# Kernel optimization log

Hardware: AMD Instinct MI355X
Metric: run time of the kernel (lower is better)

Reference implementation:

```python
import jax, jax.numpy as jnp
import numpy as np

B, N, DIM, HEADS, DEPTH, MLP = 4, 1024, 256, 4, 4, 1024
DH = DIM // HEADS
EPS = 1e-5


def _ln(x, g, b):
    mu = jnp.mean(x, axis=-1, keepdims=True)
    var = jnp.mean((x - mu) ** 2, axis=-1, keepdims=True)
    return (x - mu) / jnp.sqrt(var + EPS) * g + b


def setup_inputs() -> dict:
    key = jax.random.key(0)
    ks = jax.random.split(key, 10)
    s = 0.02
    p = {}
    p["x"] = jax.random.normal(ks[0], (B, N, DIM), jnp.float32)
    p["attn_bias"] = jax.random.normal(ks[1], (2, B, HEADS, N, N), jnp.float32)
    p["ln1_g"] = jnp.ones((DEPTH, DIM), jnp.float32)
    p["ln1_b"] = jnp.zeros((DEPTH, DIM), jnp.float32)
    p["Wkv"] = jax.random.normal(ks[2], (DEPTH, DIM, 2 * DIM), jnp.float32) * s
    p["Wq"] = jax.random.normal(ks[3], (DEPTH, DIM, DIM), jnp.float32) * s
    p["Wo"] = jax.random.normal(ks[4], (DEPTH, DIM, DIM), jnp.float32) * s
    p["bo"] = jnp.zeros((DEPTH, DIM), jnp.float32)
    p["ln2_g"] = jnp.ones((DEPTH, DIM), jnp.float32)
    p["ln2_b"] = jnp.zeros((DEPTH, DIM), jnp.float32)
    p["W1"] = jax.random.normal(ks[5], (DEPTH, DIM, MLP), jnp.float32) * s
    p["b1"] = jnp.zeros((DEPTH, MLP), jnp.float32)
    p["W2"] = jax.random.normal(ks[6], (DEPTH, MLP, DIM), jnp.float32) * s
    p["b2"] = jnp.zeros((DEPTH, DIM), jnp.float32)
    p["Wg"] = jax.random.normal(ks[7], (DIM, DIM), jnp.float32) * s
    p["lng_g"] = jnp.ones((DIM,), jnp.float32)
    p["lng_b"] = jnp.zeros((DIM,), jnp.float32)
    return p


def reference(x, attn_bias, ln1_g, ln1_b, Wkv, Wq, Wo, bo, ln2_g, ln2_b, W1, b1, W2, b2, Wg, lng_g, lng_b):
    scale = DIM ** -0.5
    add_attn = attn_bias[0] + attn_bias[1]            # [B,H,N,N]
    # aggregation bias matrices are layer-invariant (recomputed identically each layer in torch)
    A = jnp.mean(attn_bias[0], axis=1)                # [B,N,N]
    S = jnp.mean(attn_bias[1], axis=1)
    G = jax.nn.softmax(A * S, axis=2)                 # [B,N,N]

    def split_heads(t):  # [B,N,DIM] -> [B,H,N,DH]
        return t.reshape(B, N, HEADS, DH).transpose(0, 2, 1, 3)

    for l in range(DEPTH):
        # softmax-GCN aggregation
        x_ma = jax.nn.relu(_ln(jnp.matmul(G, x) @ Wg, lng_g, lng_b))
        # attention (PreNorm on x only; q comes from un-normed x_ma)
        xn = _ln(x, ln1_g[l], ln1_b[l])
        kv = xn @ Wkv[l]
        k, v = jnp.split(kv, 2, axis=-1)
        q = x_ma @ Wq[l]
        qh, kh, vh = split_heads(q), split_heads(k), split_heads(v)
        dots = jnp.einsum('bhid,bhjd->bhij', qh, kh) * scale + add_attn
        attn = jax.nn.softmax(dots, axis=-1)
        out = jnp.einsum('bhij,bhjd->bhid', attn, vh)
        out = out.transpose(0, 2, 1, 3).reshape(B, N, DIM)
        x = x + out @ Wo[l] + bo[l]
        # feed-forward (exact GELU, matching torch nn.GELU default)
        xn2 = _ln(x, ln2_g[l], ln2_b[l])
        x = x + jax.nn.gelu(xn2 @ W1[l] + b1[l], approximate=False) @ W2[l] + b2[l]
    return x
```

## Files before the change

### kernel.cpp

```cpp
#include <hip/hip_runtime.h>
#include <hip/hip_bf16.h>
#include <math.h>

typedef unsigned short u16;
typedef __bf16 bf16x8 __attribute__((ext_vector_type(8)));
typedef float f32x4 __attribute__((ext_vector_type(4)));

#define B_ 4
#define N_ 1024
#define DIM_ 256
#define HEADS_ 4
#define DH_ 64
#define MLP_ 1024
#define DEPTH_ 4

__device__ __forceinline__ float r2f(u16 r){ return __uint_as_float(((unsigned)r)<<16); }
__device__ __forceinline__ u16 f2r(float f){ __hip_bfloat16 h = __float2bfloat16(f); return *(u16*)&h; }
__device__ __forceinline__ void stv(float* p, float v){ *p = v; }
__device__ __forceinline__ void stv(u16* p, float v){ *p = f2r(v); }

__device__ __forceinline__ float gelu_exact(float v){
  return 0.5f*v*(1.0f + erff(v*0.70710678118654752440f));
}

#define MFMA16(a,b,c) __builtin_amdgcn_mfma_f32_16x16x32_bf16(a,b,c,0,0,0)

__global__ void prep_bias(const float* __restrict__ bias, u16* __restrict__ G, u16* __restrict__ bsum){
  int blk = blockIdx.x;
  int i = blk & (N_-1);
  int b = blk >> 10;
  int t = threadIdx.x;
  __shared__ float sc[N_];
  __shared__ float red[256];
  long long base0 = ((long long)(b*HEADS_)*N_ + i)*(long long)N_;
  const long long hs = (long long)N_*N_;
  const long long cs = (long long)B_*HEADS_*N_*N_;
  float lmax = -3e38f;
  for (int jj=0;jj<4;jj++){
    int j = t + jj*256;
    float a = 0.f, s = 0.f;
    #pragma unroll
    for (int h=0;h<HEADS_;h++){
      float x0 = bias[base0 + h*hs + j];
      float x1 = bias[cs + base0 + h*hs + j];
      a += x0; s += x1;
      bsum[base0 + h*hs + j] = f2r(x0 + x1);
    }
    float v = (a*0.25f)*(s*0.25f);
    sc[j] = v;
    lmax = fmaxf(lmax, v);
  }
  red[t]=lmax; __syncthreads();
  for (int s=128;s>0;s>>=1){ if(t<s) red[t]=fmaxf(red[t],red[t+s]); __syncthreads(); }
  float m = red[0]; __syncthreads();
  float lsum = 0.f;
  for (int jj=0;jj<4;jj++){
    int j = t + jj*256;
    float e = __expf(sc[j]-m);
    sc[j]=e; lsum+=e;
  }
  red[t]=lsum; __syncthreads();
  for (int s=128;s>0;s>>=1){ if(t<s) red[t]+=red[t+s]; __syncthreads(); }
  float inv = 1.0f/red[0];
  u16* Grow = G + ((long long)b*N_ + i)*(long long)N_;
  for (int jj=0;jj<4;jj++){ int j=t+jj*256; Grow[j]=f2r(sc[j]*inv); }
}

__global__ void ln_kernel(const float* __restrict__ X, u16* __restrict__ Y,
                          const float* __restrict__ g, const float* __restrict__ bvec){
  int row = blockIdx.x, t = threadIdx.x;
  __shared__ float red[256];
  float v = X[(long long)row*DIM_ + t];
  red[t]=v; __syncthreads();
  for (int s=128;s>0;s>>=1){ if(t<s) red[t]+=red[t+s]; __syncthreads(); }
  float mu = red[0]*(1.0f/DIM_); __syncthreads();
  float d = v - mu;
  red[t]=d*d; __syncthreads();
  for (int s=128;s>0;s>>=1){ if(t<s) red[t]+=red[t+s]; __syncthreads(); }
  float var = red[0]*(1.0f/DIM_);
  Y[(long long)row*DIM_ + t] = f2r(d*rsqrtf(var+1e-5f)*g[t] + bvec[t]);
}

__global__ void tcast_all(const float* __restrict__ Wkv, const float* __restrict__ Wq,
                          const float* __restrict__ Wo, const float* __restrict__ W1,
                          const float* __restrict__ W2, const float* __restrict__ Wg,
                          const float* __restrict__ xin,
                          u16* WkvT, u16* WqT, u16* WoT, u16* W1T, u16* W2T, u16* WgT, u16* xT){
  int z = blockIdx.z;
  const float* I; u16* O; int ldin, R, C;
  if (z < 4)       { I = Wkv + z*131072;      O = WkvT + z*131072;      ldin=512;  R=256;  C=512;  }
  else if (z < 8)  { I = Wq  + (z-4)*65536;   O = WqT  + (z-4)*65536;   ldin=256;  R=256;  C=256;  }
  else if (z < 12) { I = Wo  + (z-8)*65536;   O = WoT  + (z-8)*65536;   ldin=256;  R=256;  C=256;  }
  else if (z < 16) { I = W1  + (z-12)*262144; O = W1T  + (z-12)*262144; ldin=1024; R=256;  C=1024; }
  else if (z < 20) { I = W2  + (z-16)*262144; O = W2T  + (z-16)*262144; ldin=256;  R=1024; C=256;  }
  else if (z == 20){ I = Wg;                  O = WgT;                  ldin=256;  R=256;  C=256;  }
  else             { I = xin + (z-21)*262144; O = xT   + (z-21)*262144; ldin=256;  R=1024; C=256;  }
  int c0 = blockIdx.x*32, r0 = blockIdx.y*32;
  if (c0 >= C || r0 >= R) return;
  __shared__ float tile[32][33];
  int tx = threadIdx.x, ty = threadIdx.y;
  #pragma unroll
  for (int i=0;i<4;i++)
    tile[ty*4+i][tx] = I[(long long)(r0+ty*4+i)*ldin + c0+tx];
  __syncthreads();
  #pragma unroll
  for (int i=0;i<4;i++)
    O[(long long)(c0+ty*4+i)*R + r0+tx] = f2r(tile[tx][ty*4+i]);
}

template<typename OT, int ACT>
__global__ __launch_bounds__(256) void wgemm(
    const u16* __restrict__ A, const u16* __restrict__ BT, OT* __restrict__ Cb,
    int K, int lda, int ldbt, int ldc, int ZS,
    long long sAb, long long sAh, long long sBb, long long sBh,
    long long sCb, long long sCh,
    const float* __restrict__ colBias, const float* __restrict__ res,
    u16* __restrict__ vt)
{
  int z = blockIdx.z, zb = z>>ZS, zh = z & ((1<<ZS)-1);
  A  += zb*sAb + zh*sAh;
  BT += zb*sBb + zh*sBh;
  long long co = zb*sCb + zh*sCh;
  int tid = threadIdx.x, w = tid>>6, lane = tid&63;
  int lr = lane&15, qd = lane>>4;
  int m0 = blockIdx.y*64 + (w>>1)*32;
  int n0 = blockIdx.x*64 + (w&1)*32;
  const u16* Ap0 = A  + (long long)(m0+lr)*lda;
  const u16* Ap1 = A  + (long long)(m0+16+lr)*lda;
  const u16* Bp0 = BT + (long long)(n0+lr)*ldbt;
  const u16* Bp1 = BT + (long long)(n0+16+lr)*ldbt;
  f32x4 acc[2][2] = {};
  for (int k0=0; k0<K; k0+=64){
    #pragma unroll
    for (int ks=0; ks<2; ks++){
      int ko = k0 + ks*32 + qd*8;
      bf16x8 a0 = *(const bf16x8*)(Ap0+ko);
      bf16x8 a1 = *(const bf16x8*)(Ap1+ko);
      bf16x8 b0 = *(const bf16x8*)(Bp0+ko);
      bf16x8 b1 = *(const bf16x8*)(Bp1+ko);
      acc[0][0] = MFMA16(a0,b0,acc[0][0]);
      acc[0][1] = MFMA16(a0,b1,acc[0][1]);
      acc[1][0] = MFMA16(a1,b0,acc[1][0]);
      acc[1][1] = MFMA16(a1,b1,acc[1][1]);
    }
  }
  OT* C = Cb + co;
  const float* rs = res ? res + co : nullptr;
  #pragma unroll
  for (int rt=0;rt<2;rt++){
    #pragma unroll
    for (int ct=0;ct<2;ct++){
      int gc = n0 + ct*16 + lr;
      float cb = colBias ? colBias[gc] : 0.f;
      #pragma unroll
      for (int r=0;r<4;r++){
        int gr = m0 + rt*16 + qd*4 + r;
        float v = acc[rt][ct][r] + cb;
        if (ACT) v = gelu_exact(v);
        if (rs) v += rs[(long long)gr*ldc + gc];
        stv(C + (long long)gr*ldc + gc, v);
        if (vt && gc >= 256){
          int b = gr>>10, rl = gr&1023;
          vt[(long long)b*262144 + (long long)(gc-256)*1024 + rl] = f2r(v);
        }
      }
    }
  }
}

static inline void gemm(hipStream_t st, const u16* A, const u16* BT, void* C, int outBf, int act,
    int M, int N, int K, int lda, int ldbt, int ldc, int Z, int ZS,
    long long sAb, long long sAh, long long sBb, long long sBh, long long sCb, long long sCh,
    const float* cb, const float* res, u16* vt)
{
  dim3 g(N/64, M/64, Z), b(256);
  if (outBf){
    if (act) wgemm<u16,1><<<g,b,0,st>>>(A,BT,(u16*)C,K,lda,ldbt,ldc,ZS,sAb,sAh,sBb,sBh,sCb,sCh,cb,res,vt);
    else     wgemm<u16,0><<<g,b,0,st>>>(A,BT,(u16*)C,K,lda,ldbt,ldc,ZS,sAb,sAh,sBb,sBh,sCb,sCh,cb,res,vt);
  } else {
    if (act) wgemm<float,1><<<g,b,0,st>>>(A,BT,(float*)C,K,lda,ldbt,ldc,ZS,sAb,sAh,sBb,sBh,sCb,sCh,cb,res,vt);
    else     wgemm<float,0><<<g,b,0,st>>>(A,BT,(float*)C,K,lda,ldbt,ldc,ZS,sAb,sAh,sBb,sBh,sCb,sCh,cb,res,vt);
  }
}

template<int MODE>
__global__ __launch_bounds__(64) void gemmln(
    const u16* __restrict__ A, const u16* __restrict__ BT, int K, int ldbt,
    const float* __restrict__ colBias, const float* __restrict__ res,
    float* __restrict__ fout,
    const float* __restrict__ lng, const float* __restrict__ lnb,
    u16* __restrict__ lnOut, u16* __restrict__ xTout)
{
  int lane = threadIdx.x;
  int lr = lane&15, qd = lane>>4;
  int m0 = blockIdx.x*16;
  const u16* Ap = A + (long long)(m0+lr)*K;
  f32x4 acc[16] = {};
  for (int k0=0;k0<K;k0+=32){
    bf16x8 af = *(const bf16x8*)(Ap + k0 + qd*8);
    #pragma unroll
    for (int ct=0;ct<16;ct++){
      bf16x8 bfv = *(const bf16x8*)(BT + (long long)(ct*16+lr)*ldbt + k0 + qd*8);
      acc[ct] = MFMA16(af, bfv, acc[ct]);
    }
  }
  #pragma unroll
  for (int r=0;r<4;r++){
    int row = m0 + qd*4 + r;
    float v[16];
    #pragma unroll
    for (int ct=0;ct<16;ct++){
      float x = acc[ct][r];
      if (MODE>=1){ int col = ct*16+lr; x += colBias[col] + res[(long long)row*DIM_ + col]; }
      v[ct] = x;
    }
    if (MODE>=1){
      #pragma unroll
      for (int ct=0;ct<16;ct++) fout[(long long)row*DIM_ + ct*16+lr] = v[ct];
    }
    if (MODE==2 && xTout){
      int b = row>>10, rl = row&1023;
      #pragma unroll
      for (int ct=0;ct<16;ct++)
        xTout[(long long)b*262144 + (long long)(ct*16+lr)*1024 + rl] = f2r(v[ct]);
    }
    if (MODE==0 || lnOut){
      float s=0.f;
      #pragma unroll
      for (int ct=0;ct<16;ct++) s += v[ct];
      s += __shfl_xor(s,1); s += __shfl_xor(s,2); s += __shfl_xor(s,4); s += __shfl_xor(s,8);
      float mu = s*(1.0f/256.0f);
      float s2=0.f;
      #pragma unroll
      for (int ct=0;ct<16;ct++){ float d=v[ct]-mu; s2 += d*d; }
      s2 += __shfl_xor(s2,1); s2 += __shfl_xor(s2,2); s2 += __shfl_xor(s2,4); s2 += __shfl_xor(s2,8);
      float rstd = rsqrtf(s2*(1.0f/256.0f)+1e-5f);
      #pragma unroll
      for (int ct=0;ct<16;ct++){
        int col = ct*16+lr;
        float y = (v[ct]-mu)*rstd*lng[col] + lnb[col];
        if (MODE==0) y = fmaxf(y,0.f);
        lnOut[(long long)row*DIM_ + col] = f2r(y);
      }
    }
  }
}

__global__ __launch_bounds__(256) void flash_attn(
    const u16* __restrict__ qb, const u16* __restrict__ kvb,
    const u16* __restrict__ vt, const u16* __restrict__ bsum,
    u16* __restrict__ out)
{
  int z = blockIdx.z;
  int b = z>>2, h = z&3;
  int qt = blockIdx.x;
  int tid = threadIdx.x;
  int w = tid>>6, lane = tid&63;
  int lr = lane&15, qd = lane>>4;
  __shared__ u16 Pl[4][16][72];
  __shared__ u16 sb[4][16][72];

  int qrow0 = qt*64 + w*16;
  const u16* qp = qb + ((long long)(b*N_) + qrow0 + lr)*DIM_ + h*DH_;
  bf16x8 aq0 = *(const bf16x8*)(qp + qd*8);
  bf16x8 aq1 = *(const bf16x8*)(qp + 32 + qd*8);

  f32x4 oacc[4] = {};
  float m_r[4] = {-3e38f,-3e38f,-3e38f,-3e38f};
  float l_r[4] = {0.f,0.f,0.f,0.f};

  const u16* kbase = kvb + ((long long)(b*N_))*512 + h*DH_;
  const u16* vbase = vt + (long long)b*(DIM_*N_) + (long long)(h*DH_)*N_;
  const u16* bias_base = bsum + ((long long)z*N_ + qrow0)*(long long)N_;
  int srr = lane>>2, scc = (lane&3)*16;

  for (int jt=0; jt<16; jt++){
    int j0 = jt*64;
    {
      const u16* gs = bias_base + (long long)srr*N_ + j0 + scc;
      uint4 t0 = *(const uint4*)gs;
      uint4 t1 = *(const uint4*)(gs+8);
      *(uint4*)&sb[w][srr][scc]   = t0;
      *(uint4*)&sb[w][srr][scc+8] = t1;
    }
    f32x4 sacc[4] = {};
    #pragma unroll
    for (int nt=0; nt<4; nt++){
      const u16* kp = kbase + (long long)(j0 + nt*16 + lr)*512;
      bf16x8 bk0 = *(const bf16x8*)(kp + qd*8);
      bf16x8 bk1 = *(const bf16x8*)(kp + 32 + qd*8);
      sacc[nt] = MFMA16(aq0, bk0, sacc[nt]);
      sacc[nt] = MFMA16(aq1, bk1, sacc[nt]);
    }
    #pragma unroll
    for (int r=0;r<4;r++){
      float pv[4];
      float vmax = -3e38f;
      #pragma unroll
      for (int nt=0;nt<4;nt++){
        float v = sacc[nt][r]*0.0625f + r2f(sb[w][qd*4+r][nt*16+lr]);
        pv[nt] = v;
        vmax = fmaxf(vmax, v);
      }
      vmax = fmaxf(vmax, __shfl_xor(vmax,1));
      vmax = fmaxf(vmax, __shfl_xor(vmax,2));
      vmax = fmaxf(vmax, __shfl_xor(vmax,4));
      vmax = fmaxf(vmax, __shfl_xor(vmax,8));
      float newm = fmaxf(m_r[r], vmax);
      float alpha = __expf(m_r[r]-newm);
      m_r[r] = newm;
      float psum = 0.f;
      #pragma unroll
      for (int nt=0;nt<4;nt++){
        float p = __expf(pv[nt]-newm);
        psum += p;
        Pl[w][qd*4+r][nt*16+lr] = f2r(p);
      }
      psum += __shfl_xor(psum,1);
      psum += __shfl_xor(psum,2);
      psum += __shfl_xor(psum,4);
      psum += __shfl_xor(psum,8);
      l_r[r] = l_r[r]*alpha + psum;
      #pragma unroll
      for (int ot=0;ot<4;ot++) oacc[ot][r] *= alpha;
    }
    #pragma unroll
    for (int ks=0;ks<2;ks++){
      bf16x8 ap = *(const bf16x8*)&Pl[w][lr][ks*32 + qd*8];
      #pragma unroll
      for (int ot=0;ot<4;ot++){
        const u16* vp = vbase + (long long)(ot*16+lr)*N_ + j0 + ks*32 + qd*8;
        bf16x8 bv = *(const bf16x8*)vp;
        oacc[ot] = MFMA16(ap, bv, oacc[ot]);
      }
    }
  }
  #pragma unroll
  for (int r=0;r<4;r++){
    float inv = 1.0f/l_r[r];
    #pragma unroll
    for (int ot=0;ot<4;ot++){
      out[((long long)(b*N_) + qrow0 + qd*4 + r)*DIM_ + h*DH_ + ot*16 + lr]
          = f2r(oacc[ot][r]*inv);
    }
  }
}

extern "C" void kernel_launch(void* const* d_in, const int* in_sizes, int n_in,
                              void* d_out, int out_size, void* d_ws, size_t ws_size,
                              hipStream_t stream){
  const float* x_in   = (const float*)d_in[0];
  const float* abias  = (const float*)d_in[1];
  const float* ln1_g  = (const float*)d_in[2];
  const float* ln1_b  = (const float*)d_in[3];
  const float* Wkv    = (const float*)d_in[4];
  const float* Wq     = (const float*)d_in[5];
  const float* Wo     = (const float*)d_in[6];
  const float* bo     = (const float*)d_in[7];
  const float* ln2_g  = (const float*)d_in[8];
  const float* ln2_b  = (const float*)d_in[9];
  const float* W1     = (const float*)d_in[10];
  const float* b1     = (const float*)d_in[11];
  const float* W2     = (const float*)d_in[12];
  const float* b2     = (const float*)d_in[13];
  const float* Wg     = (const float*)d_in[14];
  const float* lng_g  = (const float*)d_in[15];
  const float* lng_b  = (const float*)d_in[16];

  char* ws = (char*)d_ws;
  float* xf   = (float*)(ws);
  u16*  Gb    = (u16*)(ws + (4ll<<20));
  u16*  bsum  = (u16*)(ws + (12ll<<20));
  u16*  kvb   = (u16*)(ws + (44ll<<20));
  u16*  vt    = (u16*)(ws + (48ll<<20));
  u16*  xT    = (u16*)(ws + (50ll<<20));
  u16*  tmp1b = (u16*)(ws + (52ll<<20));
  u16*  xnb   = (u16*)(ws + (54ll<<20));
  u16*  xmab  = (u16*)(ws + (56ll<<20));
  u16*  qb    = (u16*)(ws + (58ll<<20));
  u16*  aob   = (u16*)(ws + (60ll<<20));
  u16*  h1b   = (u16*)(ws + (62ll<<20));
  u16*  WkvT  = (u16*)(ws + (70ll<<20));
  u16*  WqT   = (u16*)(ws + (71ll<<20));
  u16*  WoT   = (u16*)(ws + (71ll<<20) + (512ll<<10));
  u16*  W1T   = (u16*)(ws + (72ll<<20));
  u16*  W2T   = (u16*)(ws + (74ll<<20));
  u16*  WgT   = (u16*)(ws + (76ll<<20));

  dim3 b256(256);

  prep_bias<<<dim3(B_*N_), b256, 0, stream>>>(abias, Gb, bsum);
  tcast_all<<<dim3(32,32,25), dim3(32,8), 0, stream>>>(Wkv,Wq,Wo,W1,W2,Wg,x_in,
                                                       WkvT,WqT,WoT,W1T,W2T,WgT,xT);
  ln_kernel<<<dim3(B_*N_), b256, 0, stream>>>(x_in, xnb, ln1_g, ln1_b);

  for (int l=0; l<DEPTH_; l++){
    const float* resx = (l==0) ? x_in : xf;
    gemm(stream, Gb, xT, tmp1b, 1, 0, 1024, 256, 1024, 1024, 1024, 256, B_, 0,
         1048576,0, 262144,0, 262144,0, nullptr, nullptr, nullptr);
    gemmln<0><<<dim3(256), dim3(64), 0, stream>>>(tmp1b, WgT, 256, 256,
        nullptr, nullptr, nullptr, lng_g, lng_b, xmab, nullptr);
    gemm(stream, xnb, WkvT + (long long)l*131072, kvb, 1, 0, 4096, 512, 256, 256, 256, 512, 1, 0,
         0,0,0,0,0,0, nullptr, nullptr, vt);
    gemm(stream, xmab, WqT + (long long)l*65536, qb, 1, 0, 4096, 256, 256, 256, 256, 256, 1, 0,
         0,0,0,0,0,0, nullptr, nullptr, nullptr);
    flash_attn<<<dim3(16,1,B_*HEADS_), b256, 0, stream>>>(qb, kvb, vt, bsum, aob);
    gemmln<1><<<dim3(256), dim3(64), 0, stream>>>(aob, WoT + (long long)l*65536, 256, 256,
        bo + l*DIM_, resx, xf, ln2_g + l*DIM_, ln2_b + l*DIM_, xnb, nullptr);
    gemm(stream, xnb, W1T + (long long)l*262144, h1b, 1, 1, 4096, 1024, 256, 256, 256, 1024, 1, 0,
         0,0,0,0,0,0, b1 + l*MLP_, nullptr, nullptr);
    if (l < DEPTH_-1){
      gemmln<2><<<dim3(256), dim3(64), 0, stream>>>(h1b, W2T + (long long)l*262144, 1024, 1024,
          b2 + l*DIM_, xf, xf, ln1_g + (l+1)*DIM_, ln1_b + (l+1)*DIM_, xnb, xT);
    } else {
      gemmln<2><<<dim3(256), dim3(64), 0, stream>>>(h1b, W2T + (long long)l*262144, 1024, 1024,
          b2 + l*DIM_, xf, (float*)d_out, nullptr, nullptr, nullptr, nullptr);
    }
  }
}
```

Measured before the change: 846.6 us.

## Fuse per-layer GEMM chains into two row-block megakernels around attention

Replaces the per-layer sequence of separate GEMM and GEMM+LayerNorm launches with two fused kernels. layer_pre computes G@x (split-K across waves), the Wg projection, LayerNorm+ReLU, the Q projection and the KV projection for a 16-row block. layer_post computes the Wo projection with residual, LN2, W1 with GELU, W2 with residual and the next layer's LN1, keeping intermediates in shared memory. This removes intermediate global round-trips and launch count, at the cost of only 256 blocks of 512 threads with heavy weight rereads per block and large shared-memory footprint.

```diff
diff --git a/kernel.cpp b/kernel.cpp
--- a/kernel.cpp
+++ b/kernel.cpp
@@ -16,8 +16,6 @@
 
 __device__ __forceinline__ float r2f(u16 r){ return __uint_as_float(((unsigned)r)<<16); }
 __device__ __forceinline__ u16 f2r(float f){ __hip_bfloat16 h = __float2bfloat16(f); return *(u16*)&h; }
-__device__ __forceinline__ void stv(float* p, float v){ *p = v; }
-__device__ __forceinline__ void stv(u16* p, float v){ *p = f2r(v); }
 
 __device__ __forceinline__ float gelu_exact(float v){
   return 0.5f*v*(1.0f + erff(v*0.70710678118654752440f));
@@ -108,139 +106,123 @@
     O[(long long)(c0+ty*4+i)*R + r0+tx] = f2r(tile[tx][ty*4+i]);
 }
 
-template<typename OT, int ACT>
-__global__ __launch_bounds__(256) void wgemm(
-    const u16* __restrict__ A, const u16* __restrict__ BT, OT* __restrict__ Cb,
-    int K, int lda, int ldbt, int ldc, int ZS,
-    long long sAb, long long sAh, long long sBb, long long sBh,
-    long long sCb, long long sCh,
-    const float* __restrict__ colBias, const float* __restrict__ res,
-    u16* __restrict__ vt)
+__global__ __launch_bounds__(512) void layer_pre(
+    const u16* __restrict__ Gb, const u16* __restrict__ xT, const u16* __restrict__ xnb,
+    const u16* __restrict__ WgT, const u16* __restrict__ WqT, const u16* __restrict__ WkvT,
+    const float* __restrict__ lng, const float* __restrict__ lnb,
+    u16* __restrict__ qb, u16* __restrict__ kvb, u16* __restrict__ vt)
 {
-  int z = blockIdx.z, zb = z>>ZS, zh = z & ((1<<ZS)-1);
-  A  += zb*sAb + zh*sAh;
-  BT += zb*sBb + zh*sBh;
-  long long co = zb*sCb + zh*sCh;
-  int tid = threadIdx.x, w = tid>>6, lane = tid&63;
-  int lr = lane&15, qd = lane>>4;
-  int m0 = blockIdx.y*64 + (w>>1)*32;
-  int n0 = blockIdx.x*64 + (w&1)*32;
-  const u16* Ap0 = A  + (long long)(m0+lr)*lda;
-  const u16* Ap1 = A  + (long long)(m0+16+lr)*lda;
-  const u16* Bp0 = BT + (long long)(n0+lr)*ldbt;
-  const u16* Bp1 = BT + (long long)(n0+16+lr)*ldbt;
-  f32x4 acc[2][2] = {};
-  for (int k0=0; k0<K; k0+=64){
-    #pragma unroll
-    for (int ks=0; ks<2; ks++){
-      int ko = k0 + ks*32 + qd*8;
-      bf16x8 a0 = *(const bf16x8*)(Ap0+ko);
-      bf16x8 a1 = *(const bf16x8*)(Ap1+ko);
-      bf16x8 b0 = *(const bf16x8*)(Bp0+ko);
-      bf16x8 b1 = *(const bf16x8*)(Bp1+ko);
-      acc[0][0] = MFMA16(a0,b0,acc[0][0]);
-      acc[0][1] = MFMA16(a0,b1,acc[0][1]);
-      acc[1][0] = MFMA16(a1,b0,acc[1][0]);
-      acc[1][1] = MFMA16(a1,b1,acc[1][1]);
-    }
-  }
-  OT* C = Cb + co;
-  const float* rs = res ? res + co : nullptr;
-  #pragma unroll
-  for (int rt=0;rt<2;rt++){
-    #pragma unroll
-    for (int ct=0;ct<2;ct++){
-      int gc = n0 + ct*16 + lr;
-      float cb = colBias ? colBias[gc] : 0.f;
+  __shared__ float Gx_s[16][264];
+  __shared__ float t2_s[16][264];
+  __shared__ u16  xma_s[16][264];
+  int tid = threadIdx.x;
+  int w = tid>>6, lane = tid&63, lr = lane&15, qd = lane>>4;
+  int row0 = blockIdx.x*16;
+  int batch = row0>>10, brow0 = row0&1023;
+
+  {
+    int kw = w>>2, cw = w&3;
+    const u16* Ap = Gb + (long long)batch*1048576 + (long long)(brow0+lr)*1024 + kw*512;
+    const u16* Bp = xT + (long long)batch*262144 + (long long)kw*512;
+    f32x4 acc[4] = {};
+    for (int k0=0;k0<512;k0+=32){
+      bf16x8 af = *(const bf16x8*)(Ap + k0 + qd*8);
+      #pragma unroll
+      for (int nt=0;nt<4;nt++){
+        bf16x8 bf = *(const bf16x8*)(Bp + (long long)(cw*64+nt*16+lr)*1024 + k0 + qd*8);
+        acc[nt] = MFMA16(af,bf,acc[nt]);
+      }
+    }
+    if (kw==0){
+      #pragma unroll
+      for (int nt=0;nt<4;nt++)
+        #pragma unroll
+        for (int r=0;r<4;r++) Gx_s[qd*4+r][cw*64+nt*16+lr] = acc[nt][r];
+    }
+    __syncthreads();
+    if (kw==1){
+      #pragma unroll
+      for (int nt=0;nt<4;nt++)
+        #pragma unroll
+        for (int r=0;r<4;r++) Gx_s[qd*4+r][cw*64+nt*16+lr] += acc[nt][r];
+    }
+    __syncthreads();
+  }
+  {
+    f32x4 acc[2] = {};
+    for (int k0=0;k0<256;k0+=32){
+      bf16x8 af;
+      #pragma unroll
+      for (int i=0;i<8;i++) af[i] = (__bf16)Gx_s[lr][k0+qd*8+i];
+      #pragma unroll
+      for (int i=0;i<2;i++){
+        bf16x8 bf = *(const bf16x8*)(WgT + (long long)((w*2+i)*16+lr)*256 + k0 + qd*8);
+        acc[i] = MFMA16(af,bf,acc[i]);
+      }
+    }
+    #pragma unroll
+    for (int i=0;i<2;i++)
+      #pragma unroll
+      for (int r=0;r<4;r++) t2_s[qd*4+r][(w*2+i)*16+lr] = acc[i][r];
+  }
+  __syncthreads();
+  {
+    int r = tid>>5, cg = tid&31;
+    float v[8]; float s=0.f;
+    #pragma unroll
+    for (int i=0;i<8;i++){ v[i] = t2_s[r][cg*8+i]; s += v[i]; }
+    s += __shfl_xor(s,1); s += __shfl_xor(s,2); s += __shfl_xor(s,4); s += __shfl_xor(s,8); s += __shfl_xor(s,16);
+    float mu = s*(1.0f/256.0f);
+    float s2=0.f;
+    #pragma unroll
+    for (int i=0;i<8;i++){ float d=v[i]-mu; s2 += d*d; }
+    s2 += __shfl_xor(s2,1); s2 += __shfl_xor(s2,2); s2 += __shfl_xor(s2,4); s2 += __shfl_xor(s2,8); s2 += __shfl_xor(s2,16);
+    float rstd = rsqrtf(s2*(1.0f/256.0f)+1e-5f);
+    #pragma unroll
+    for (int i=0;i<8;i++){
+      int c = cg*8+i;
+      float y = (v[i]-mu)*rstd*lng[c] + lnb[c];
+      xma_s[r][c] = f2r(fmaxf(y,0.f));
+    }
+  }
+  __syncthreads();
+  {
+    f32x4 acc[2] = {};
+    for (int k0=0;k0<256;k0+=32){
+      bf16x8 af = *(const bf16x8*)&xma_s[lr][k0+qd*8];
+      #pragma unroll
+      for (int i=0;i<2;i++){
+        bf16x8 bf = *(const bf16x8*)(WqT + (long long)((w*2+i)*16+lr)*256 + k0 + qd*8);
+        acc[i] = MFMA16(af,bf,acc[i]);
+      }
+    }
+    #pragma unroll
+    for (int i=0;i<2;i++)
+      #pragma unroll
+      for (int r=0;r<4;r++)
+        qb[(long long)(row0+qd*4+r)*DIM_ + (w*2+i)*16+lr] = f2r(acc[i][r]);
+  }
+  {
+    const u16* Ap = xnb + (long long)(row0+lr)*DIM_;
+    f32x4 acc[4] = {};
+    for (int k0=0;k0<256;k0+=32){
+      bf16x8 af = *(const bf16x8*)(Ap + k0 + qd*8);
+      #pragma unroll
+      for (int i=0;i<4;i++){
+        bf16x8 bf = *(const bf16x8*)(WkvT + (long long)((w*4+i)*16+lr)*256 + k0 + qd*8);
+        acc[i] = MFMA16(af,bf,acc[i]);
+      }
+    }
+    #pragma unroll
+    for (int i=0;i<4;i++){
+      int col = (w*4+i)*16+lr;
       #pragma unroll
       for (int r=0;r<4;r++){
-        int gr = m0 + rt*16 + qd*4 + r;
-        float v = acc[rt][ct][r] + cb;
-        if (ACT) v = gelu_exact(v);
-        if (rs) v += rs[(long long)gr*ldc + gc];
-        stv(C + (long long)gr*ldc + gc, v);
-        if (vt && gc >= 256){
-          int b = gr>>10, rl = gr&1023;
-          vt[(long long)b*262144 + (long long)(gc-256)*1024 + rl] = f2r(v);
-        }
-      }
-    }
-  }
-}
-
-static inline void gemm(hipStream_t st, const u16* A, const u16* BT, void* C, int outBf, int act,
-    int M, int N, int K, int lda, int ldbt, int ldc, int Z, int ZS,
-    long long sAb, long long sAh, long long sBb, long long sBh, long long sCb, long long sCh,
-    const float* cb, const float* res, u16* vt)
-{
-  dim3 g(N/64, M/64, Z), b(256);
-  if (outBf){
-    if (act) wgemm<u16,1><<<g,b,0,st>>>(A,BT,(u16*)C,K,lda,ldbt,ldc,ZS,sAb,sAh,sBb,sBh,sCb,sCh,cb,res,vt);
-    else     wgemm<u16,0><<<g,b,0,st>>>(A,BT,(u16*)C,K,lda,ldbt,ldc,ZS,sAb,sAh,sBb,sBh,sCb,sCh,cb,res,vt);
-  } else {
-    if (act) wgemm<float,1><<<g,b,0,st>>>(A,BT,(float*)C,K,lda,ldbt,ldc,ZS,sAb,sAh,sBb,sBh,sCb,sCh,cb,res,vt);
-    else     wgemm<float,0><<<g,b,0,st>>>(A,BT,(float*)C,K,lda,ldbt,ldc,ZS,sAb,sAh,sBb,sBh,sCb,sCh,cb,res,vt);
-  }
-}
-
-template<int MODE>
-__global__ __launch_bounds__(64) void gemmln(
-    const u16* __restrict__ A, const u16* __restrict__ BT, int K, int ldbt,
-    const float* __restrict__ colBias, const float* __restrict__ res,
-    float* __restrict__ fout,
-    const float* __restrict__ lng, const float* __restrict__ lnb,
-    u16* __restrict__ lnOut, u16* __restrict__ xTout)
-{
-  int lane = threadIdx.x;
-  int lr = lane&15, qd = lane>>4;
-  int m0 = blockIdx.x*16;
-  const u16* Ap = A + (long long)(m0+lr)*K;
-  f32x4 acc[16] = {};
-  for (int k0=0;k0<K;k0+=32){
-    bf16x8 af = *(const bf16x8*)(Ap + k0 + qd*8);
-    #pragma unroll
-    for (int ct=0;ct<16;ct++){
-      bf16x8 bfv = *(const bf16x8*)(BT + (long long)(ct*16+lr)*ldbt + k0 + qd*8);
-      acc[ct] = MFMA16(af, bfv, acc[ct]);
-    }
-  }
-  #pragma unroll
-  for (int r=0;r<4;r++){
-    int row = m0 + qd*4 + r;
-    float v[16];
-    #pragma unroll
-    for (int ct=0;ct<16;ct++){
-      float x = acc[ct][r];
-      if (MODE>=1){ int col = ct*16+lr; x += colBias[col] + res[(long long)row*DIM_ + col]; }
-      v[ct] = x;
-    }
-    if (MODE>=1){
-      #pragma unroll
-      for (int ct=0;ct<16;ct++) fout[(long long)row*DIM_ + ct*16+lr] = v[ct];
-    }
-    if (MODE==2 && xTout){
-      int b = row>>10, rl = row&1023;
-      #pragma unroll
-      for (int ct=0;ct<16;ct++)
-        xTout[(long long)b*262144 + (long long)(ct*16+lr)*1024 + rl] = f2r(v[ct]);
-    }
-    if (MODE==0 || lnOut){
-      float s=0.f;
-      #pragma unroll
-      for (int ct=0;ct<16;ct++) s += v[ct];
-      s += __shfl_xor(s,1); s += __shfl_xor(s,2); s += __shfl_xor(s,4); s += __shfl_xor(s,8);
-      float mu = s*(1.0f/256.0f);
-      float s2=0.f;
-      #pragma unroll
-      for (int ct=0;ct<16;ct++){ float d=v[ct]-mu; s2 += d*d; }
-      s2 += __shfl_xor(s2,1); s2 += __shfl_xor(s2,2); s2 += __shfl_xor(s2,4); s2 += __shfl_xor(s2,8);
-      float rstd = rsqrtf(s2*(1.0f/256.0f)+1e-5f);
-      #pragma unroll
-      for (int ct=0;ct<16;ct++){
-        int col = ct*16+lr;
-        float y = (v[ct]-mu)*rstd*lng[col] + lnb[col];
-        if (MODE==0) y = fmaxf(y,0.f);
-        lnOut[(long long)row*DIM_ + col] = f2r(y);
+        int row = row0+qd*4+r;
+        float v = acc[i][r];
+        kvb[(long long)row*512 + col] = f2r(v);
+        if (col >= 256)
+          vt[(long long)batch*262144 + (long long)(col-256)*1024 + (row&1023)] = f2r(v);
       }
     }
   }
@@ -342,6 +324,127 @@
     for (int ot=0;ot<4;ot++){
       out[((long long)(b*N_) + qrow0 + qd*4 + r)*DIM_ + h*DH_ + ot*16 + lr]
           = f2r(oacc[ot][r]*inv);
+    }
+  }
+}
+
+__global__ __launch_bounds__(512) void layer_post(
+    const u16* __restrict__ aob, const float* __restrict__ resx,
+    const u16* __restrict__ WoT, const float* __restrict__ bo,
+    const float* __restrict__ ln2g, const float* __restrict__ ln2b,
+    const u16* __restrict__ W1T, const float* __restrict__ b1,
+    const u16* __restrict__ W2T, const float* __restrict__ b2,
+    float* __restrict__ xf_out,
+    const float* __restrict__ ln1g_next, const float* __restrict__ ln1b_next,
+    u16* __restrict__ xn_out, u16* __restrict__ xT_out)
+{
+  __shared__ float v_s[16][264];
+  __shared__ u16  xn2_s[16][264];
+  __shared__ u16  h1_s[16][1048];
+  __shared__ float xnew_s[16][264];
+  int tid = threadIdx.x;
+  int w = tid>>6, lane = tid&63, lr = lane&15, qd = lane>>4;
+  int row0 = blockIdx.x*16;
+  int batch = row0>>10;
+
+  {
+    const u16* Ap = aob + (long long)(row0+lr)*DIM_;
+    f32x4 acc[2] = {};
+    for (int k0=0;k0<256;k0+=32){
+      bf16x8 af = *(const bf16x8*)(Ap + k0 + qd*8);
+      #pragma unroll
+      for (int i=0;i<2;i++){
+        bf16x8 bf = *(const bf16x8*)(WoT + (long long)((w*2+i)*16+lr)*256 + k0 + qd*8);
+        acc[i] = MFMA16(af,bf,acc[i]);
+      }
+    }
+    #pragma unroll
+    for (int i=0;i<2;i++){
+      int col = (w*2+i)*16+lr;
+      #pragma unroll
+      for (int r=0;r<4;r++)
+        v_s[qd*4+r][col] = acc[i][r] + bo[col] + resx[(long long)(row0+qd*4+r)*DIM_ + col];
+    }
+  }
+  __syncthreads();
+  {
+    int r = tid>>5, cg = tid&31;
+    float v[8]; float s=0.f;
+    #pragma unroll
+    for (int i=0;i<8;i++){ v[i] = v_s[r][cg*8+i]; s += v[i]; }
+    s += __shfl_xor(s,1); s += __shfl_xor(s,2); s += __shfl_xor(s,4); s += __shfl_xor(s,8); s += __shfl_xor(s,16);
+    float mu = s*(1.0f/256.0f);
+    float s2=0.f;
+    #pragma unroll
+    for (int i=0;i<8;i++){ float d=v[i]-mu; s2 += d*d; }
+    s2 += __shfl_xor(s2,1); s2 += __shfl_xor(s2,2); s2 += __shfl_xor(s2,4); s2 += __shfl_xor(s2,8); s2 += __shfl_xor(s2,16);
+    float rstd = rsqrtf(s2*(1.0f/256.0f)+1e-5f);
+    #pragma unroll
+    for (int i=0;i<8;i++){
+      int c = cg*8+i;
+      xn2_s[r][c] = f2r((v[i]-mu)*rstd*ln2g[c] + ln2b[c]);
+    }
+  }
+  __syncthreads();
+  {
+    f32x4 acc[8] = {};
+    for (int k0=0;k0<256;k0+=32){
+      bf16x8 af = *(const bf16x8*)&xn2_s[lr][k0+qd*8];
+      #pragma unroll
+      for (int i=0;i<8;i++){
+        bf16x8 bf = *(const bf16x8*)(W1T + (long long)((w*8+i)*16+lr)*256 + k0 + qd*8);
+        acc[i] = MFMA16(af,bf,acc[i]);
+      }
+    }
+    #pragma unroll
+    for (int i=0;i<8;i++){
+      int col = (w*8+i)*16+lr;
+      #pragma unroll
+      for (int r=0;r<4;r++)
+        h1_s[qd*4+r][col] = f2r(gelu_exact(acc[i][r] + b1[col]));
+    }
+  }
+  __syncthreads();
+  {
+    f32x4 acc[2] = {};
+    for (int k0=0;k0<1024;k0+=32){
+      bf16x8 af = *(const bf16x8*)&h1_s[lr][k0+qd*8];
+      #pragma unroll
+      for (int i=0;i<2;i++){
+        bf16x8 bf = *(const bf16x8*)(W2T + (long long)((w*2+i)*16+lr)*1024 + k0 + qd*8);
+        acc[i] = MFMA16(af,bf,acc[i]);
+      }
+    }
+    #pragma unroll
+    for (int i=0;i<2;i++){
+      int col = (w*2+i)*16+lr;
+      #pragma unroll
+      for (int r=0;r<4;r++){
+        float v = acc[i][r] + b2[col] + v_s[qd*4+r][col];
+        xf_out[(long long)(row0+qd*4+r)*DIM_ + col] = v;
+        xnew_s[qd*4+r][col] = v;
+      }
+    }
+  }
+  if (ln1g_next){
+    __syncthreads();
+    int r = tid>>5, cg = tid&31;
+    float v[8]; float s=0.f;
+    #pragma unroll
+    for (int i=0;i<8;i++){ v[i] = xnew_s[r][cg*8+i]; s += v[i]; }
+    s += __shfl_xor(s,1); s += __shfl_xor(s,2); s += __shfl_xor(s,4); s += __shfl_xor(s,8); s += __shfl_xor(s,16);
+    float mu = s*(1.0f/256.0f);
+    float s2=0.f;
+    #pragma unroll
+    for (int i=0;i<8;i++){ float d=v[i]-mu; s2 += d*d; }
+    s2 += __shfl_xor(s2,1); s2 += __shfl_xor(s2,2); s2 += __shfl_xor(s2,4); s2 += __shfl_xor(s2,8); s2 += __shfl_xor(s2,16);
+    float rstd = rsqrtf(s2*(1.0f/256.0f)+1e-5f);
+    int grow = row0 + r;
+    #pragma unroll
+    for (int i=0;i<8;i++){
+      int c = cg*8+i;
+      xn_out[(long long)grow*DIM_ + c] = f2r((v[i]-mu)*rstd*ln1g_next[c] + ln1b_next[c]);
+      xT_out[(long long)batch*262144 + (long long)c*1024 + (grow&1023)] = f2r(v[i]);
     }
   }
 }
@@ -374,20 +477,17 @@
   u16*  kvb   = (u16*)(ws + (44ll<<20));
   u16*  vt    = (u16*)(ws + (48ll<<20));
   u16*  xT    = (u16*)(ws + (50ll<<20));
-  u16*  tmp1b = (u16*)(ws + (52ll<<20));
-  u16*  xnb   = (u16*)(ws + (54ll<<20));
-  u16*  xmab  = (u16*)(ws + (56ll<<20));
-  u16*  qb    = (u16*)(ws + (58ll<<20));
-  u16*  aob   = (u16*)(ws + (60ll<<20));
-  u16*  h1b   = (u16*)(ws + (62ll<<20));
-  u16*  WkvT  = (u16*)(ws + (70ll<<20));
-  u16*  WqT   = (u16*)(ws + (71ll<<20));
-  u16*  WoT   = (u16*)(ws + (71ll<<20) + (512ll<<10));
-  u16*  W1T   = (u16*)(ws + (72ll<<20));
-  u16*  W2T   = (u16*)(ws + (74ll<<20));
-  u16*  WgT   = (u16*)(ws + (76ll<<20));
-
-  dim3 b256(256);
+  u16*  xnb   = (u16*)(ws + (52ll<<20));
+  u16*  qb    = (u16*)(ws + (54ll<<20));
+  u16*  aob   = (u16*)(ws + (56ll<<20));
+  u16*  WkvT  = (u16*)(ws + (58ll<<20));
+  u16*  WqT   = (u16*)(ws + (59ll<<20));
+  u16*  WoT   = (u16*)(ws + (59ll<<20) + (512ll<<10));
+  u16*  W1T   = (u16*)(ws + (60ll<<20));
+  u16*  W2T   = (u16*)(ws + (62ll<<20));
+  u16*  WgT   = (u16*)(ws + (64ll<<20));
+
+  dim3 b256(256), b512(512);
 
   prep_bias<<<dim3(B_*N_), b256, 0, stream>>>(abias, Gb, bsum);
   tcast_all<<<dim3(32,32,25), dim3(32,8), 0, stream>>>(Wkv,Wq,Wo,W1,W2,Wg,x_in,
@@ -396,25 +496,20 @@
 
   for (int l=0; l<DEPTH_; l++){
     const float* resx = (l==0) ? x_in : xf;
-    gemm(stream, Gb, xT, tmp1b, 1, 0, 1024, 256, 1024, 1024, 1024, 256, B_, 0,
-         1048576,0, 262144,0, 262144,0, nullptr, nullptr, nullptr);
-    gemmln<0><<<dim3(256), dim3(64), 0, stream>>>(tmp1b, WgT, 256, 256,
-        nullptr, nullptr, nullptr, lng_g, lng_b, xmab, nullptr);
-    gemm(stream, xnb, WkvT + (long long)l*131072, kvb, 1, 0, 4096, 512, 256, 256, 256, 512, 1, 0,
-         0,0,0,0,0,0, nullptr, nullptr, vt);
-    gemm(stream, xmab, WqT + (long long)l*65536, qb, 1, 0, 4096, 256, 256, 256, 256, 256, 1, 0,
-         0,0,0,0,0,0, nullptr, nullptr, nullptr);
+    layer_pre<<<dim3(256), b512, 0, stream>>>(Gb, xT, xnb,
+        WgT, WqT + (long long)l*65536, WkvT + (long long)l*131072,
+        lng_g, lng_b, qb, kvb, vt);
     flash_attn<<<dim3(16,1,B_*HEADS_), b256, 0, stream>>>(qb, kvb, vt, bsum, aob);
-    gemmln<1><<<dim3(256), dim3(64), 0, stream>>>(aob, WoT + (long long)l*65536, 256, 256,
-        bo + l*DIM_, resx, xf, ln2_g + l*DIM_, ln2_b + l*DIM_, xnb, nullptr);
-    gemm(stream, xnb, W1T + (long long)l*262144, h1b, 1, 1, 4096, 1024, 256, 256, 256, 1024, 1, 0,
-         0,0,0,0,0,0, b1 + l*MLP_, nullptr, nullptr);
     if (l < DEPTH_-1){
-      gemmln<2><<<dim3(256), dim3(64), 0, stream>>>(h1b, W2T + (long long)l*262144, 1024, 1024,
-          b2 + l*DIM_, xf, xf, ln1_g + (l+1)*DIM_, ln1_b + (l+1)*DIM_, xnb, xT);
+      layer_post<<<dim3(256), b512, 0, stream>>>(aob, resx,
+          WoT + (long long)l*65536, bo + l*DIM_, ln2_g + l*DIM_, ln2_b + l*DIM_,
+          W1T + (long long)l*262144, b1 + l*MLP_, W2T + (long long)l*262144, b2 + l*DIM_,
+          xf, ln1_g + (l+1)*DIM_, ln1_b + (l+1)*DIM_, xnb, xT);
     } else {
-      gemmln<2><<<dim3(256), dim3(64), 0, stream>>>(h1b, W2T + (long long)l*262144, 1024, 1024,
-          b2 + l*DIM_, xf, (float*)d_out, nullptr, nullptr, nullptr, nullptr);
-    }
-  }
-}
+      layer_post<<<dim3(256), b512, 0, stream>>>(aob, resx,
+          WoT + (long long)l*65536, bo + l*DIM_, ln2_g + l*DIM_, ln2_b + l*DIM_,
+          W1T + (long long)l*262144, b1 + l*MLP_, W2T + (long long)l*262144, b2 + l*DIM_,
+          (float*)d_out, nullptr, nullptr, nullptr, nullptr);
+    }
+  }
+}
```

Result: faster. 731.0 us (-13.7%).
